# Performance work log

Hardware: AMD Instinct MI355X
Metric: run time of the kernel (lower is better)

The kernel has to match this reference:

```python
import jax, jax.numpy as jnp
import numpy as np

B, S, F, E = 8, 2048, 512, 512

def setup_inputs() -> dict:
    key = jax.random.key(0)
    k1, k2, k3, k4 = jax.random.split(key, 4)
    x = jax.random.normal(k1, (B, S, F), dtype=jnp.float32)
    # nn.Linear(feat, embed, bias=False): y = x @ W.T; store W as [F, E] already transposed
    scale = 1.0 / np.sqrt(F)
    Wq = jax.random.uniform(k2, (F, E), dtype=jnp.float32, minval=-scale, maxval=scale)
    Wk = jax.random.uniform(k3, (F, E), dtype=jnp.float32, minval=-scale, maxval=scale)
    Wv = jax.random.uniform(k4, (F, E), dtype=jnp.float32, minval=-scale, maxval=scale)
    return {"x": x, "Wq": Wq, "Wk": Wk, "Wv": Wv}

def reference(x, Wq, Wk, Wv):
    # QKV projections: [B, S, E]
    Q = jnp.einsum('bsf,fe->bse', x, Wq)
    K = jnp.einsum('bsf,fe->bse', x, Wk)
    V = jnp.einsum('bsf,fe->bse', x, Wv)
    # scores: [B, S, S], scaled by sqrt(E)
    scores = jnp.einsum('bqe,bke->bqk', Q, K) / jnp.sqrt(jnp.asarray(Q.shape[-1], Q.dtype))
    attn = jax.nn.softmax(scores, axis=-1)
    return jnp.einsum('bqk,bke->bqe', attn, V)
```

## Files before the change

### kernel.cpp

```cpp
#include <hip/hip_runtime.h>
#include <hip/hip_bf16.h>
#include <stdint.h>

#define B_ 8
#define S_ 2048
#define F_ 512
#define E_ 512

typedef short bf16x8 __attribute__((ext_vector_type(8)));
typedef float f32x4 __attribute__((ext_vector_type(4)));

__device__ __forceinline__ f32x4 mfma16(bf16x8 a, bf16x8 b, f32x4 c) {
  return __builtin_amdgcn_mfma_f32_16x16x32_bf16(a, b, c, 0, 0, 0);
}

__device__ __forceinline__ void gll16(const void* g, void* l) {
  __builtin_amdgcn_global_load_lds(
      (const __attribute__((address_space(1))) void*)g,
      (__attribute__((address_space(3))) void*)l, 16, 0, 0);
}

constexpr float QSCALE = 0.0441941738f * 1.44269504f;

__global__ void xconv_kernel(const float* __restrict__ x,
                             __hip_bfloat16* __restrict__ xb) {
  int i = (blockIdx.x * 256 + threadIdx.x) * 8;
  float4 a = *(const float4*)(x + i);
  float4 b = *(const float4*)(x + i + 4);
  union { __hip_bfloat16 h[8]; uint4 u; } cv;
  cv.h[0] = __float2bfloat16(a.x);
  cv.h[1] = __float2bfloat16(a.y);
  cv.h[2] = __float2bfloat16(a.z);
  cv.h[3] = __float2bfloat16(a.w);
  cv.h[4] = __float2bfloat16(b.x);
  cv.h[5] = __float2bfloat16(b.y);
  cv.h[6] = __float2bfloat16(b.z);
  cv.h[7] = __float2bfloat16(b.w);
  *(uint4*)(xb + i) = cv.u;
}

__global__ void wtrans_kernel(const float* __restrict__ wq,
                              const float* __restrict__ wk,
                              const float* __restrict__ wv,
                              __hip_bfloat16* __restrict__ wt) {
  __shared__ float t[32][33];
  const float* w = (blockIdx.z == 0) ? wq : (blockIdx.z == 1 ? wk : wv);
  __hip_bfloat16* o = wt + (size_t)blockIdx.z * F_ * E_;
  int e0 = blockIdx.x * 32, f0 = blockIdx.y * 32;
  int tx = threadIdx.x, ty = threadIdx.y;
#pragma unroll
  for (int i = 0; i < 4; i++)
    t[ty + 8 * i][tx] = w[(size_t)(f0 + ty + 8 * i) * E_ + e0 + tx];
  __syncthreads();
#pragma unroll
  for (int i = 0; i < 4; i++)
    o[(size_t)(e0 + ty + 8 * i) * F_ + f0 + tx] = __float2bfloat16(t[tx][ty + 8 * i]);
}

__global__ __launch_bounds__(256, 2) void qkvg_kernel(
    const __hip_bfloat16* __restrict__ xb, const __hip_bfloat16* __restrict__ wt,
    __hip_bfloat16* __restrict__ Qb, __hip_bfloat16* __restrict__ Kb,
    __hip_bfloat16* __restrict__ Vt) {
  __shared__ __hip_bfloat16 Al[2][128][64] __attribute__((aligned(16)));
  __shared__ __hip_bfloat16 Bl[2][128][64] __attribute__((aligned(16)));

  int tid = threadIdx.x;
  int lane = tid & 63, w = tid >> 6;
  int el = lane & 15, g = lane >> 4;
  int r7 = el & 7;
  int m0 = blockIdx.x * 128, n0 = blockIdx.y * 128, z = blockIdx.z;
  const __hip_bfloat16* wz = wt + (size_t)z * F_ * E_;
  int wr = w >> 1, wc = w & 1;

  int srcoff = (((lane & 7) ^ ((lane >> 3) & 7)) << 3);
  auto stage = [&](int kk, int bf) {
#pragma unroll
    for (int i = 0; i < 4; i++) {
      gll16(xb + (size_t)(m0 + w * 32 + i * 8 + (lane >> 3)) * F_ + kk * 64 + srcoff,
            &Al[bf][w * 32 + i * 8][0]);
      gll16(wz + (size_t)(n0 + w * 32 + i * 8 + (lane >> 3)) * F_ + kk * 64 + srcoff,
            &Bl[bf][w * 32 + i * 8][0]);
    }
  };

  f32x4 acc[4][4] = {};
  stage(0, 0);
  asm volatile("s_waitcnt vmcnt(0)" ::: "memory");
  __syncthreads();

  for (int kk = 0; kk < 8; ++kk) {
    int bf = kk & 1;
    if (kk < 7) stage(kk + 1, bf ^ 1);
#pragma unroll
    for (int ks = 0; ks < 2; ++ks) {
      bf16x8 av[4], bv[4];
#pragma unroll
      for (int mi = 0; mi < 4; mi++)
        av[mi] = *(const bf16x8*)((const char*)&Al[bf][0][0] +
                                  (wr * 64 + mi * 16 + el) * 128 +
                                  (((ks * 4 + g) ^ r7) << 4));
#pragma unroll
      for (int ni = 0; ni < 4; ni++)
        bv[ni] = *(const bf16x8*)((const char*)&Bl[bf][0][0] +
                                  (wc * 64 + ni * 16 + el) * 128 +
                                  (((ks * 4 + g) ^ r7) << 4));
#pragma unroll
      for (int mi = 0; mi < 4; mi++)
#pragma unroll
        for (int ni = 0; ni < 4; ni++)
          acc[mi][ni] = mfma16(av[mi], bv[ni], acc[mi][ni]);
    }
    asm volatile("s_waitcnt vmcnt(0)" ::: "memory");
    __syncthreads();
  }

  float sc = (z == 0) ? QSCALE : 1.0f;
#pragma unroll
  for (int mi = 0; mi < 4; mi++)
#pragma unroll
    for (int ni = 0; ni < 4; ni++) {
      int mB = m0 + wr * 64 + mi * 16 + g * 4;
      int n = n0 + wc * 64 + ni * 16 + el;
      if (z == 2) {
        union { __hip_bfloat16 h[4]; uint2 u; } pk;
#pragma unroll
        for (int r = 0; r < 4; r++) pk.h[r] = __float2bfloat16(acc[mi][ni][r]);
        int b = mB >> 11, sl = mB & 2047;
        *(uint2*)&Vt[(size_t)b * E_ * S_ + (size_t)n * S_ + sl] = pk.u;
      } else {
#pragma unroll
        for (int r = 0; r < 4; r++) {
          __hip_bfloat16 v = __float2bfloat16(acc[mi][ni][r] * sc);
          if (z == 0) Qb[(size_t)(mB + r) * E_ + n] = v;
          else Kb[(size_t)(mB + r) * E_ + n] = v;
        }
      }
    }
}

__global__ __launch_bounds__(256, 2) void qkv_kernel(
    const float* __restrict__ x, const __hip_bfloat16* __restrict__ wt,
    __hip_bfloat16* __restrict__ Qb, __hip_bfloat16* __restrict__ Kb,
    __hip_bfloat16* __restrict__ Vt) {
  __shared__ __hip_bfloat16 Al[2][128][72];
  __shared__ __hip_bfloat16 Bl[2][128][72];
  int tid = threadIdx.x;
  int lane = tid & 63, w = tid >> 6;
  int el = lane & 15, g = lane >> 4;
  int m0 = blockIdx.x * 128, n0 = blockIdx.y * 128, z = blockIdx.z;
  const __hip_bfloat16* wz = wt + (size_t)z * F_ * E_;
  int wr = w >> 1, wc = w & 1;
  float4 fa[8];
  uint4 vb[4];
  auto load = [&](int kk) {
#pragma unroll
    for (int c = 0; c < 4; c++) {
      int id = tid + 256 * c;
      int row = id >> 3, k8 = (id & 7) * 8;
      const float* s = x + (size_t)(m0 + row) * F_ + kk * 64 + k8;
      fa[2 * c] = *(const float4*)s;
      fa[2 * c + 1] = *(const float4*)(s + 4);
      vb[c] = *(const uint4*)(wz + (size_t)(n0 + row) * F_ + kk * 64 + k8);
    }
  };
  auto store_lds = [&](int bf) {
#pragma unroll
    for (int c = 0; c < 4; c++) {
      int id = tid + 256 * c;
      int row = id >> 3, k8 = (id & 7) * 8;
      union { __hip_bfloat16 h[8]; uint4 u; } cv;
      cv.h[0] = __float2bfloat16(fa[2 * c].x);
      cv.h[1] = __float2bfloat16(fa[2 * c].y);
      cv.h[2] = __float2bfloat16(fa[2 * c].z);
      cv.h[3] = __float2bfloat16(fa[2 * c].w);
      cv.h[4] = __float2bfloat16(fa[2 * c + 1].x);
      cv.h[5] = __float2bfloat16(fa[2 * c + 1].y);
      cv.h[6] = __float2bfloat16(fa[2 * c + 1].z);
      cv.h[7] = __float2bfloat16(fa[2 * c + 1].w);
      *(uint4*)&Al[bf][row][k8] = cv.u;
      *(uint4*)&Bl[bf][row][k8] = vb[c];
    }
  };
  f32x4 acc[4][4] = {};
  load(0);
  store_lds(0);
  __syncthreads();
  for (int kk = 0; kk < 8; ++kk) {
    int bf = kk & 1;
    if (kk < 7) load(kk + 1);
#pragma unroll
    for (int ks = 0; ks < 2; ++ks) {
      bf16x8 av[4], bv[4];
#pragma unroll
      for (int mi = 0; mi < 4; mi++)
        av[mi] = *(const bf16x8*)((const char*)&Al[bf][0][0] +
                                  (wr * 64 + mi * 16 + el) * 144 + (ks * 32 + g * 8) * 2);
#pragma unroll
      for (int ni = 0; ni < 4; ni++)
        bv[ni] = *(const bf16x8*)((const char*)&Bl[bf][0][0] +
                                  (wc * 64 + ni * 16 + el) * 144 + (ks * 32 + g * 8) * 2);
#pragma unroll
      for (int mi = 0; mi < 4; mi++)
#pragma unroll
        for (int ni = 0; ni < 4; ni++)
          acc[mi][ni] = mfma16(av[mi], bv[ni], acc[mi][ni]);
    }
    if (kk < 7) store_lds(bf ^ 1);
    __syncthreads();
  }
  float sc = (z == 0) ? QSCALE : 1.0f;
#pragma unroll
  for (int mi = 0; mi < 4; mi++)
#pragma unroll
    for (int ni = 0; ni < 4; ni++)
#pragma unroll
      for (int r = 0; r < 4; r++) {
        int m = m0 + wr * 64 + mi * 16 + g * 4 + r;
        int n = n0 + wc * 64 + ni * 16 + el;
        __hip_bfloat16 v = __float2bfloat16(acc[mi][ni][r] * sc);
        if (z == 0) Qb[(size_t)m * E_ + n] = v;
        else if (z == 1) Kb[(size_t)m * E_ + n] = v;
        else {
          int b = m >> 11, sl = m & 2047;
          Vt[(size_t)b * E_ * S_ + (size_t)n * S_ + sl] = v;
        }
      }
}

template <int MODE>
__global__ __launch_bounds__(256, MODE ? 2 : 1) void attn_kernel(
    const __hip_bfloat16* __restrict__ Qb, const __hip_bfloat16* __restrict__ Kb,
    const __hip_bfloat16* __restrict__ Vt, float* __restrict__ out,
    __hip_bfloat16* __restrict__ part0, __hip_bfloat16* __restrict__ part1,
    float* __restrict__ Ls, float* __restrict__ Ms) {
  __shared__ __hip_bfloat16 Kl[32][512] __attribute__((aligned(16)));
  __shared__ __hip_bfloat16 Vl[512][32] __attribute__((aligned(16)));
  __shared__ __hip_bfloat16 Pl[4][16][40] __attribute__((aligned(16)));

  int tid = threadIdx.x;
  int lane = tid & 63, w = tid >> 6;
  int el = lane & 15, g = lane >> 4, x7 = lane & 7;
  int bx = blockIdx.x;
  int batch = bx & 7, qt = (bx >> 3) & 31;
  int half = MODE ? (bx >> 8) : 0;
  int nt = MODE ? 32 : 64;
  int tbase = half * 32;
  int q0 = qt * 64 + w * 16;

  bf16x8 qf[16];
  {
    const __hip_bfloat16* qptr = Qb + (size_t)(batch * S_ + q0 + el) * E_ + g * 8;
#pragma unroll
    for (int s = 0; s < 16; s++) qf[s] = *(const bf16x8*)(qptr + 32 * s);
  }

  f32x4 o[32] = {};
  float m_run = -INFINITY, l_run = 0.f;

  const char* kbase_g = (const char*)(Kb + (size_t)batch * S_ * E_);
  const char* vbase_g = (const char*)(Vt + (size_t)batch * E_ * S_);
  int vsrc_lane = (lane >> 2) * (S_ * 2) + 16 * ((lane & 3) ^ ((lane >> 3) & 3));

  auto stage = [&](int t) {
#pragma unroll
    for (int i = 0; i < 8; i++) {
      int row = w * 8 + i;
      const char* src =
          kbase_g + ((size_t)(t * 32 + row) * 512 + 8 * (lane ^ i)) * 2;
      gll16(src, &Kl[row][0]);
    }
#pragma unroll
    for (int i = 0; i < 8; i++) {
      int eb = (w * 8 + i) * 16;
      const char* src = vbase_g + (size_t)eb * (S_ * 2) + vsrc_lane + t * 64;
      gll16(src, &Vl[eb][0]);
    }
  };

  int ka0 = el * 1024 + ((g ^ x7) << 4);
  int ka1 = el * 1024 + (((4 + g) ^ x7) << 4);
  int vbase_l = el * 64 + ((g ^ ((el >> 1) & 3)) << 4);

  stage(tbase);
  asm volatile("s_waitcnt vmcnt(0)" ::: "memory");
  __syncthreads();

  for (int i = 0; i < nt; ++i) {
    const char* kl = (const char*)&Kl[0][0];
    f32x4 st[2] = {};
    __builtin_amdgcn_s_setprio(1);
#pragma unroll
    for (int s = 0; s < 16; s++) {
      int base = ((s & 1) ? ka1 : ka0) + (s >> 1) * 128;
#pragma unroll
      for (int f = 0; f < 2; f++) {
        bf16x8 kf = *(const bf16x8*)(kl + base + f * 16384);
        st[f] = mfma16(kf, qf[s], st[f]);
      }
    }
    __builtin_amdgcn_s_setprio(0);
    float vmax = st[0][0];
#pragma unroll
    for (int r = 1; r < 4; r++) vmax = fmaxf(vmax, st[0][r]);
#pragma unroll
    for (int r = 0; r < 4; r++) vmax = fmaxf(vmax, st[1][r]);
    vmax = fmaxf(vmax, __shfl_xor(vmax, 16));
    vmax = fmaxf(vmax, __shfl_xor(vmax, 32));
    if (__any(vmax > m_run + 8.0f)) {
      float m_new = fmaxf(m_run, vmax);
      float fac = exp2f(m_run - m_new);
      float fo[4];
#pragma unroll
      for (int r = 0; r < 4; r++) fo[r] = __shfl(fac, g * 4 + r);
#pragma unroll
      for (int ni = 0; ni < 32; ni++) {
        o[ni][0] *= fo[0]; o[ni][1] *= fo[1]; o[ni][2] *= fo[2]; o[ni][3] *= fo[3];
      }
      l_run *= fac;
      m_run = m_new;
    }
    float p[8];
    float rs = 0.f;
#pragma unroll
    for (int f = 0; f < 2; f++)
#pragma unroll
      for (int r = 0; r < 4; r++) {
        float e2 = exp2f(st[f][r] - m_run);
        p[4 * f + r] = e2;
        rs += e2;
      }
    rs += __shfl_xor(rs, 16);
    rs += __shfl_xor(rs, 32);
    l_run += rs;
#pragma unroll
    for (int f = 0; f < 2; f++) {
      union { __hip_bfloat16 h[4]; uint2 u; } pk;
      pk.h[0] = __float2bfloat16(p[4 * f + 0]);
      pk.h[1] = __float2bfloat16(p[4 * f + 1]);
      pk.h[2] = __float2bfloat16(p[4 * f + 2]);
      pk.h[3] = __float2bfloat16(p[4 * f + 3]);
      *(uint2*)((char*)&Pl[w][0][0] + el * 80 + 32 * f + 8 * g) = pk.u;
    }
    asm volatile("s_waitcnt lgkmcnt(0)" ::: "memory");
    bf16x8 pa = *(const bf16x8*)((const char*)&Pl[w][0][0] + el * 80 + g * 16);
    asm volatile("s_waitcnt vmcnt(0)" ::: "memory");
    __syncthreads();
    const char* vl = (const char*)&Vl[0][0];
    __builtin_amdgcn_s_setprio(1);
#pragma unroll
    for (int ni = 0; ni < 32; ni++) {
      bf16x8 vf = *(const bf16x8*)(vl + vbase_l + ni * 1024);
      o[ni] = mfma16(pa, vf, o[ni]);
    }
    __builtin_amdgcn_s_setprio(0);
    __syncthreads();
    if (i + 1 < nt) {
      stage(tbase + i + 1);
      asm volatile("s_waitcnt vmcnt(8)" ::: "memory");
      __syncthreads();
    }
  }

  if (MODE == 0) {
    float linv[4];
#pragma unroll
    for (int r = 0; r < 4; r++) {
      float lr = __shfl(l_run, g * 4 + r);
      linv[r] = 1.0f / lr;
    }
    float* ob = out + (size_t)(batch * S_ + q0 + g * 4) * E_ + el;
#pragma unroll
    for (int ni = 0; ni < 32; ni++)
#pragma unroll
      for (int r = 0; r < 4; r++)
        ob[(size_t)r * E_ + ni * 16] = o[ni][r] * linv[r];
  } else {
    __hip_bfloat16* dst = (half == 0) ? part0 : part1;
    __hip_bfloat16* ob = dst + (size_t)(batch * S_ + q0 + g * 4) * E_ + el;
#pragma unroll
    for (int ni = 0; ni < 32; ni++)
#pragma unroll
      for (int r = 0; r < 4; r++)
        ob[(size_t)r * E_ + ni * 16] = __float2bfloat16(o[ni][r]);
    if (g == 0) {
      int idx = half * (B_ * S_) + batch * S_ + q0 + el;
      Ls[idx] = l_run;
      Ms[idx] = m_run;
    }
  }
}

__global__ void merge_kernel(float* __restrict__ out,
                             const __hip_bfloat16* __restrict__ p0,
                             const __hip_bfloat16* __restrict__ p1,
                             const float* __restrict__ Ls,
                             const float* __restrict__ Ms) {
  int idx = blockIdx.x * 256 + threadIdx.x;
  int row = idx >> 6;
  int c8 = (idx & 63) * 8;
  float l0 = Ls[row], m0 = Ms[row];
  float l1 = Ls[B_ * S_ + row], m1 = Ms[B_ * S_ + row];
  float m = fmaxf(m0, m1);
  float w0 = exp2f(m0 - m), w1 = exp2f(m1 - m);
  float inv = 1.0f / (l0 * w0 + l1 * w1);
  size_t off = (size_t)row * E_ + c8;
  union { uint4 u; ushort h[8]; } ua, ub;
  ua.u = *(const uint4*)(p0 + off);
  ub.u = *(const uint4*)(p1 + off);
  float r[8];
#pragma unroll
  for (int j = 0; j < 8; j++) {
    union { uint32_t u; float f; } a, b;
    a.u = (uint32_t)ua.h[j] << 16;
    b.u = (uint32_t)ub.h[j] << 16;
    r[j] = (a.f * w0 + b.f * w1) * inv;
  }
  *(float4*)(out + off) = *(float4*)&r[0];
  *(float4*)(out + off + 4) = *(float4*)&r[4];
}

extern "C" void kernel_launch(void* const* d_in, const int* in_sizes, int n_in,
                              void* d_out, int out_size, void* d_ws, size_t ws_size,
                              hipStream_t stream) {
  const float* x = (const float*)d_in[0];
  const float* wq = (const float*)d_in[1];
  const float* wk = (const float*)d_in[2];
  const float* wv = (const float*)d_in[3];
  float* out = (float*)d_out;

  char* ws = (char*)d_ws;
  __hip_bfloat16* wt = (__hip_bfloat16*)ws;
  __hip_bfloat16* Qb = (__hip_bfloat16*)(ws + (size_t)3 * F_ * E_ * 2);
  __hip_bfloat16* Kb = Qb + (size_t)B_ * S_ * E_;
  __hip_bfloat16* Vt = Kb + (size_t)B_ * S_ * E_;
  __hip_bfloat16* xb = Vt + (size_t)B_ * S_ * E_;
  __hip_bfloat16* part0 = xb + (size_t)B_ * S_ * F_;
  __hip_bfloat16* part1 = part0 + (size_t)B_ * S_ * E_;
  float* Ls = (float*)(part1 + (size_t)B_ * S_ * E_);
  float* Ms = Ls + 2 * B_ * S_;

  size_t need_bfx = (size_t)3 * F_ * E_ * 2 + (size_t)3 * B_ * S_ * E_ * 2 +
                    (size_t)B_ * S_ * F_ * 2;
  size_t need_split = need_bfx + (size_t)2 * B_ * S_ * E_ * 2 + 4 * B_ * S_ * 4;
  bool bfx = (ws_size >= need_bfx);
  bool split = (ws_size >= need_split);

  dim3 b0(32, 8), g0(16, 16, 3);
  wtrans_kernel<<<g0, b0, 0, stream>>>(wq, wk, wv, wt);

  dim3 g1(128, 4, 3);
  if (bfx) {
    xconv_kernel<<<(B_ * S_ * F_) / (256 * 8), 256, 0, stream>>>(x, xb);
    qkvg_kernel<<<g1, 256, 0, stream>>>(xb, wt, Qb, Kb, Vt);
  } else {
    qkv_kernel<<<g1, 256, 0, stream>>>(x, wt, Qb, Kb, Vt);
  }

  if (split) {
    attn_kernel<1><<<512, 256, 0, stream>>>(Qb, Kb, Vt, out, part0, part1, Ls, Ms);
    merge_kernel<<<(B_ * S_ * E_ / 8) / 256, 256, 0, stream>>>(out, part0, part1, Ls, Ms);
  } else {
    attn_kernel<0><<<256, 256, 0, stream>>>(Qb, Kb, Vt, out, nullptr, nullptr,
                                            nullptr, nullptr);
  }
}
```

Baseline: 181.3 us.

## Double-buffer K/V tiles and use 8-wave blocks sharing each staged tile

Attention blocks grow from 4 to 8 waves, so each staged K/V tile serves 128 queries instead of 64, which halves global and LDS staging traffic per query. K and V LDS buffers are double-buffered, and the next tile's load is issued at the start of each iteration. This lets the load overlap the QK and PV MFMA work and removes one barrier per iteration. In exchange, LDS use roughly doubles (about 130KB), so occupancy may drop. Launch bounds change to 512 threads with 2 blocks requested, which may force register pressure on the large o[32] accumulator.

```diff
diff --git a/kernel.cpp b/kernel.cpp
--- a/kernel.cpp
+++ b/kernel.cpp
@@ -228,24 +228,25 @@
 }
 
 template <int MODE>
-__global__ __launch_bounds__(256, MODE ? 2 : 1) void attn_kernel(
+__global__ __launch_bounds__(512, 2) void attn_kernel(
     const __hip_bfloat16* __restrict__ Qb, const __hip_bfloat16* __restrict__ Kb,
     const __hip_bfloat16* __restrict__ Vt, float* __restrict__ out,
     __hip_bfloat16* __restrict__ part0, __hip_bfloat16* __restrict__ part1,
     float* __restrict__ Ls, float* __restrict__ Ms) {
-  __shared__ __hip_bfloat16 Kl[32][512] __attribute__((aligned(16)));
-  __shared__ __hip_bfloat16 Vl[512][32] __attribute__((aligned(16)));
-  __shared__ __hip_bfloat16 Pl[4][16][40] __attribute__((aligned(16)));
+  __shared__ __hip_bfloat16 Kl[2][32][512] __attribute__((aligned(16)));
+  __shared__ __hip_bfloat16 Vl[2][512][32] __attribute__((aligned(16)));
+  __shared__ __hip_bfloat16 Pl[8][16][40] __attribute__((aligned(16)));
 
   int tid = threadIdx.x;
   int lane = tid & 63, w = tid >> 6;
   int el = lane & 15, g = lane >> 4, x7 = lane & 7;
   int bx = blockIdx.x;
-  int batch = bx & 7, qt = (bx >> 3) & 31;
-  int half = MODE ? (bx >> 8) : 0;
+  int batch = bx & 7;
+  int qt = MODE ? ((bx >> 3) & 15) : (bx >> 3);
+  int half = MODE ? (bx >> 7) : 0;
   int nt = MODE ? 32 : 64;
   int tbase = half * 32;
-  int q0 = qt * 64 + w * 16;
+  int q0 = qt * 128 + w * 16;
 
   bf16x8 qf[16];
   {
@@ -261,19 +262,19 @@
   const char* vbase_g = (const char*)(Vt + (size_t)batch * E_ * S_);
   int vsrc_lane = (lane >> 2) * (S_ * 2) + 16 * ((lane & 3) ^ ((lane >> 3) & 3));
 
-  auto stage = [&](int t) {
-#pragma unroll
-    for (int i = 0; i < 8; i++) {
-      int row = w * 8 + i;
+  auto stage = [&](int t, int bf) {
+#pragma unroll
+    for (int i = 0; i < 4; i++) {
+      int row = w * 4 + i;
       const char* src =
-          kbase_g + ((size_t)(t * 32 + row) * 512 + 8 * (lane ^ i)) * 2;
-      gll16(src, &Kl[row][0]);
-    }
-#pragma unroll
-    for (int i = 0; i < 8; i++) {
-      int eb = (w * 8 + i) * 16;
+          kbase_g + ((size_t)(t * 32 + row) * 512 + 8 * (lane ^ (row & 7))) * 2;
+      gll16(src, &Kl[bf][row][0]);
+    }
+#pragma unroll
+    for (int i = 0; i < 4; i++) {
+      int eb = (w * 4 + i) * 16;
       const char* src = vbase_g + (size_t)eb * (S_ * 2) + vsrc_lane + t * 64;
-      gll16(src, &Vl[eb][0]);
+      gll16(src, &Vl[bf][eb][0]);
     }
   };
 
@@ -281,12 +282,14 @@
   int ka1 = el * 1024 + (((4 + g) ^ x7) << 4);
   int vbase_l = el * 64 + ((g ^ ((el >> 1) & 3)) << 4);
 
-  stage(tbase);
+  stage(tbase, 0);
   asm volatile("s_waitcnt vmcnt(0)" ::: "memory");
   __syncthreads();
 
   for (int i = 0; i < nt; ++i) {
-    const char* kl = (const char*)&Kl[0][0];
+    int bf = i & 1;
+    if (i + 1 < nt) stage(tbase + i + 1, bf ^ 1);
+    const char* kl = (const char*)&Kl[bf][0][0];
     f32x4 st[2] = {};
     __builtin_amdgcn_s_setprio(1);
 #pragma unroll
@@ -343,9 +346,7 @@
     }
     asm volatile("s_waitcnt lgkmcnt(0)" ::: "memory");
     bf16x8 pa = *(const bf16x8*)((const char*)&Pl[w][0][0] + el * 80 + g * 16);
-    asm volatile("s_waitcnt vmcnt(0)" ::: "memory");
-    __syncthreads();
-    const char* vl = (const char*)&Vl[0][0];
+    const char* vl = (const char*)&Vl[bf][0][0];
     __builtin_amdgcn_s_setprio(1);
 #pragma unroll
     for (int ni = 0; ni < 32; ni++) {
@@ -353,12 +354,8 @@
       o[ni] = mfma16(pa, vf, o[ni]);
     }
     __builtin_amdgcn_s_setprio(0);
+    asm volatile("s_waitcnt vmcnt(0)" ::: "memory");
     __syncthreads();
-    if (i + 1 < nt) {
-      stage(tbase + i + 1);
-      asm volatile("s_waitcnt vmcnt(8)" ::: "memory");
-      __syncthreads();
-    }
   }
 
   if (MODE == 0) {
@@ -457,10 +454,10 @@
   }
 
   if (split) {
-    attn_kernel<1><<<512, 256, 0, stream>>>(Qb, Kb, Vt, out, part0, part1, Ls, Ms);
+    attn_kernel<1><<<256, 512, 0, stream>>>(Qb, Kb, Vt, out, part0, part1, Ls, Ms);
     merge_kernel<<<(B_ * S_ * E_ / 8) / 256, 256, 0, stream>>>(out, part0, part1, Ls, Ms);
   } else {
-    attn_kernel<0><<<256, 256, 0, stream>>>(Qb, Kb, Vt, out, nullptr, nullptr,
+    attn_kernel<0><<<128, 512, 0, stream>>>(Qb, Kb, Vt, out, nullptr, nullptr,
                                             nullptr, nullptr);
   }
 }
```

Result: faster. 175.6 us, median of 2 (-3.2%).
